# Performance work log

Hardware: AMD Instinct MI355X
Metric: run time of the kernel (lower is better)

Reference implementation:

```python
import jax, jax.numpy as jnp
import numpy as np

B, L, D = 64, 512, 128  # batch, word_len, dim


def setup_inputs() -> dict:
    key = jax.random.key(0)
    ks = jax.random.split(key, 12)
    p = lambda k, s: jax.random.normal(k, s, dtype=jnp.float32) * 0.05
    return {
        "EW": jax.random.normal(ks[0], (B, L, D), dtype=jnp.float32),
        "ES": jax.random.normal(ks[1], (B, L, D), dtype=jnp.float32),
        "WQ_w": p(ks[2], (D, D)), "WQ_b": p(ks[3], (D,)),
        "WK_w": p(ks[4], (D, D)), "WK_b": p(ks[5], (D,)),
        "UQ_w": p(ks[6], (D, D)), "UQ_b": p(ks[7], (D,)),
        "UK_w": p(ks[8], (D, D)), "UK_b": p(ks[9], (D,)),
        "V_w": p(ks[10], (D, D)), "V_b": p(ks[11], (D,)),
    }


def reference(EW, ES, WQ_w, WQ_b, WK_w, WK_b, UQ_w, UQ_b, UK_w, UK_b, V_w, V_b):
    dim = EW.shape[-1]
    word_len = EW.shape[-2]
    scale = 1.0 / (2.0 * dim ** 0.5)
    # word-level Q/K and sentence-level UQ/UK projections (torch Linear: x @ W.T + b)
    Q = (EW @ WQ_w.T + WQ_b) * scale   # [B, L, D]
    K = (EW @ WK_w.T + WK_b) * scale   # [B, L, D]
    UQ = (ES @ UQ_w.T + UQ_b) * scale  # [B, L, D]
    UK = (ES @ UK_w.T + UK_b) * scale  # [B, L, D]
    # two-term score matrix [B, L, L]
    alpha = jnp.einsum('bid,bjd->bij', Q, K) + jnp.einsum('bid,bjd->bij', UQ, UK)
    # manual exp/sum softmax exactly as in the source (no max subtraction;
    # denominator is broadcast along axis 1, faithful to unsqueeze(1))
    numerator = jnp.exp(alpha)                      # [B, L, L]
    denominator = numerator.sum(axis=-1)[:, None, :]  # [B, 1, L]
    soft = numerator / denominator                  # [B, L, L]
    value = EW @ V_w.T + V_b                        # [B, L, D]
    # faithful reinterpreting view (NOT a transpose): [B, L, D] -> [B, D, L]
    value = value.reshape(-1, dim, word_len)
    result = value @ soft                           # [B, D, L]
    return result.reshape(-1, word_len, dim)        # [B, L, D]
```

## Files before the change

kernel.cpp:

```cpp
#include <hip/hip_runtime.h>
#include <hip/hip_bf16.h>

#define NB 64
#define NL 512
#define ND 128
#define NK 256

typedef unsigned short ush;
typedef __attribute__((ext_vector_type(8))) short short8;
typedef __attribute__((ext_vector_type(16))) float f32x16;


__device__ __forceinline__ ush f2bs(float f) {
    union { __hip_bfloat16 h; ush u; } cv;
    cv.h = __float2bfloat16(f);
    return cv.u;
}
__device__ __forceinline__ short8 pack_bf8(float4 a, float4 b) {
    short8 r;
    r[0] = (short)f2bs(a.x); r[1] = (short)f2bs(a.y);
    r[2] = (short)f2bs(a.z); r[3] = (short)f2bs(a.w);
    r[4] = (short)f2bs(b.x); r[5] = (short)f2bs(b.y);
    r[6] = (short)f2bs(b.z); r[7] = (short)f2bs(b.w);
    return r;
}
__device__ __forceinline__ f32x16 zero16() {
    f32x16 z = {0.f,0.f,0.f,0.f,0.f,0.f,0.f,0.f,0.f,0.f,0.f,0.f,0.f,0.f,0.f,0.f};
    return z;
}

__global__ __launch_bounds__(256) void wconv_kernel(
    const float* __restrict__ W0, const float* __restrict__ W1,
    const float* __restrict__ W2, const float* __restrict__ W3,
    const float* __restrict__ W4, ush* __restrict__ Wb)
{
    const int m = blockIdx.y;
    const float* W = (m == 0) ? W0 : (m == 1) ? W1 : (m == 2) ? W2 : (m == 3) ? W3 : W4;
    const int e = (blockIdx.x * 256 + threadIdx.x) * 4;
    float4 v = *(const float4*)(W + e);
    ushort4 o;
    o.x = f2bs(v.x); o.y = f2bs(v.y); o.z = f2bs(v.z); o.w = f2bs(v.w);
    *(ushort4*)(Wb + m * 16384 + e) = o;
}

__global__ __launch_bounds__(256) void projqk_kernel(
    const float* __restrict__ EW, const float* __restrict__ ES,
    const ush* __restrict__ Wb,
    const float* __restrict__ b0, const float* __restrict__ b1,
    const float* __restrict__ b2, const float* __restrict__ b3,
    ush* __restrict__ QUf, ush* __restrict__ KUf)
{
    __shared__ ush Tls[4][2048];
    const int f = blockIdx.x;
    const int xcd = f & 7, loc = f >> 3;
    const int rt = xcd * 32 + (loc >> 2);
    const int m  = loc & 3;
    const int tid = threadIdx.x, w = tid >> 6, lane = tid & 63;
    const int l5 = lane & 31, hi = lane >> 5;
    const float* X = (m >= 2) ? ES : EW;
    const int rbase = rt * 128 + w * 32;

    const float* xr = X + (size_t)(rbase + l5) * ND + hi * 8;
    short8 af[8];
    #pragma unroll
    for (int ks = 0; ks < 8; ++ks)
        af[ks] = pack_bf8(*(const float4*)(xr + ks * 16),
                          *(const float4*)(xr + ks * 16 + 4));

    const ush* Wm = Wb + m * 16384;
    const float* Bp = (m == 0) ? b0 : (m == 1) ? b1 : (m == 2) ? b2 : b3;
    const float scl = 0.044194173824159216f;

    f32x16 acc[4];
    acc[0] = zero16(); acc[1] = zero16(); acc[2] = zero16(); acc[3] = zero16();
    #pragma unroll
    for (int ks = 0; ks < 8; ++ks) {
        #pragma unroll
        for (int nb = 0; nb < 4; ++nb) {
            short8 bf_ = *(const short8*)(Wm + (nb * 32 + l5) * 128 + ks * 16 + hi * 8);
            acc[nb] = __builtin_amdgcn_mfma_f32_32x32x16_bf16(af[ks], bf_, acc[nb], 0, 0, 0);
        }
    }

    char* Tc = (char*)Tls[w];
    ush* dstf = (m == 0 || m == 2) ? QUf : KUf;
    const int ko = (m >= 2) ? 8 : 0;
    const int p_g = rt * 4 + w;
    #pragma unroll
    for (int pass = 0; pass < 2; ++pass) {
        #pragma unroll
        for (int nbl = 0; nbl < 2; ++nbl) {
            const int nb = pass * 2 + nbl;
            float bias = Bp[nb * 32 + l5];
            #pragma unroll
            for (int r6 = 0; r6 < 16; ++r6) {
                int row = (r6 & 3) + 8 * (r6 >> 2) + 4 * hi;
                int boff = row * 128 + (((nbl * 32 + l5) * 2) ^ ((row & 7) << 4));
                *(ush*)(Tc + boff) = f2bs((acc[nb][r6] + bias) * scl);
            }
        }
        #pragma unroll
        for (int ks8 = 0; ks8 < 4; ++ks8) {
            int boff = l5 * 128 + ((ks8 * 32 + hi * 16) ^ ((l5 & 7) << 4));
            short8 v = *(const short8*)(Tc + boff);
            int ksg = ko + pass * 4 + ks8;
            *(short8*)(dstf + ((size_t)(p_g * 16 + ksg) * 64 + lane) * 8) = v;
        }
    }
}

__global__ __launch_bounds__(256) void projv_kernel(
    const float* __restrict__ EW, const ush* __restrict__ Wb,
    const float* __restrict__ b4, ush* __restrict__ Vbf)
{
    __shared__ ush lds[16384];
    const int f = blockIdx.x;
    const int rt = (f & 7) * 32 + (f >> 3);
    const int tid = threadIdx.x, w = tid >> 6, lane = tid & 63;
    const int l5 = lane & 31, hi = lane >> 5;
    const int rbase = rt * 128 + w * 32;

    const float* xr = EW + (size_t)(rbase + l5) * ND + hi * 8;
    short8 af[8];
    #pragma unroll
    for (int ks = 0; ks < 8; ++ks)
        af[ks] = pack_bf8(*(const float4*)(xr + ks * 16),
                          *(const float4*)(xr + ks * 16 + 4));

    const ush* Wm = Wb + 4 * 16384;
    f32x16 acc[4];
    acc[0] = zero16(); acc[1] = zero16(); acc[2] = zero16(); acc[3] = zero16();
    #pragma unroll
    for (int ks = 0; ks < 8; ++ks) {
        #pragma unroll
        for (int nb = 0; nb < 4; ++nb) {
            short8 bf_ = *(const short8*)(Wm + (nb * 32 + l5) * 128 + ks * 16 + hi * 8);
            acc[nb] = __builtin_amdgcn_mfma_f32_32x32x16_bf16(af[ks], bf_, acc[nb], 0, 0, 0);
        }
    }

    char* Lc = (char*)lds;
    #pragma unroll
    for (int nb = 0; nb < 4; ++nb) {
        float bias = b4[nb * 32 + l5];
        #pragma unroll
        for (int r6 = 0; r6 < 16; ++r6) {
            int row5 = (r6 & 3) + 8 * (r6 >> 2) + 4 * hi;
            int dl = w * 8 + (row5 >> 2);
            int lcol = (row5 & 3) * 128 + nb * 32 + l5;
            int boff = dl * 1024 + ((lcol * 2) ^ ((dl & 7) << 4));
            *(ush*)(Lc + boff) = f2bs(acc[nb][r6] + bias);
        }
    }
    __syncthreads();
    #pragma unroll
    for (int it = 0; it < 8; ++it) {
        int chunk = it * 256 + tid;
        int ks = chunk >> 6, ln = chunk & 63;
        int l5b = ln & 31, hib = ln >> 5;
        int boff = l5b * 1024 + ((ks * 32 + hib * 16) ^ ((l5b & 7) << 4));
        short8 v = *(const short8*)(Lc + boff);
        *(short8*)(Vbf + ((size_t)(rt * 32 + ks) * 64 + ln) * 8) = v;
    }
}

__global__ __launch_bounds__(256) void alpha_kernel(
    const ush* __restrict__ QUf, const ush* __restrict__ KUf,
    ush* __restrict__ Nf, float* __restrict__ dPart)
{
    __shared__ float red[4][2][16];
    __shared__ ush TlsA[4][2048];
    const int f = blockIdx.x;
    const int xcd = f & 7, loc = f >> 3;
    const int b  = xcd * 8 + (loc >> 5);
    const int rt = (loc >> 1) & 15;
    const int ch = loc & 1;
    const int tid = threadIdx.x, w = tid >> 6, lane = tid & 63;
    const int l5 = lane & 31, hi = lane >> 5;
    const ush* Qb = QUf + (size_t)b * 131072;
    const ush* Kb = KUf + (size_t)b * 131072;
    ush* Nfb = Nf + (size_t)b * 262144;

    const ush* qp = Qb + (size_t)rt * 8192 + lane * 8;
    const int cpg0 = ch * 8 + w * 2;

    f32x16 a0[2], a1[2];
    a0[0] = zero16(); a0[1] = zero16(); a1[0] = zero16(); a1[1] = zero16();
    #pragma unroll
    for (int ks = 0; ks < 16; ks += 2) {
        short8 aqa = *(const short8*)(qp + ks * 512);
        short8 aqb = *(const short8*)(qp + (ks + 1) * 512);
        #pragma unroll
        for (int cp = 0; cp < 2; ++cp) {
            const ush* kp = Kb + (size_t)((cpg0 + cp) * 16) * 512 + lane * 8;
            a0[cp] = __builtin_amdgcn_mfma_f32_32x32x16_bf16(aqa,
                         *(const short8*)(kp + ks * 512), a0[cp], 0, 0, 0);
            a1[cp] = __builtin_amdgcn_mfma_f32_32x32x16_bf16(aqb,
                         *(const short8*)(kp + (ks + 1) * 512), a1[cp], 0, 0, 0);
        }
    }

    float rs[16];
    #pragma unroll
    for (int r6 = 0; r6 < 16; ++r6) rs[r6] = 0.f;
    char* Tc = (char*)TlsA[w];
    #pragma unroll
    for (int cp = 0; cp < 2; ++cp) {
        const int cpg = cpg0 + cp;
        float e[16];
        #pragma unroll
        for (int r6 = 0; r6 < 16; ++r6) {
            e[r6] = __expf(a0[cp][r6] + a1[cp][r6]);
            rs[r6] += e[r6];
        }
        #pragma unroll
        for (int q = 0; q < 8; ++q) {
            int r6 = q * 2;
            int r = (r6 & 3) + 8 * (r6 >> 2) + 4 * hi;
            unsigned int pk = (unsigned int)f2bs(e[r6])
                            | ((unsigned int)f2bs(e[r6 + 1]) << 16);
            *(unsigned int*)(Tc + l5 * 128 + ((r * 2) ^ ((l5 & 7) << 4))) = pk;
        }
        #pragma unroll
        for (int ksl = 0; ksl < 2; ++ksl) {
            short8 v = *(const short8*)(Tc + l5 * 128 +
                           (((ksl * 16 + hi * 8) * 2) ^ ((l5 & 7) << 4)));
            int ksg = rt * 2 + ksl;
            *(short8*)(Nfb + ((size_t)(cpg * 32 + ksg) * 64 + lane) * 8) = v;
        }
    }

    #pragma unroll
    for (int mk = 1; mk <= 16; mk <<= 1)
        #pragma unroll
        for (int r6 = 0; r6 < 16; ++r6) rs[r6] += __shfl_xor(rs[r6], mk, 32);
    if (l5 == 0)
        #pragma unroll
        for (int r6 = 0; r6 < 16; ++r6) red[w][hi][r6] = rs[r6];
    __syncthreads();
    if (tid < 32) {
        int t = tid;
        int hh = (t >> 2) & 1, r6 = (t & 3) + 4 * (t >> 3);
        float s = red[0][hh][r6] + red[1][hh][r6] + red[2][hh][r6] + red[3][hh][r6];
        dPart[((size_t)b * 2 + ch) * NL + rt * 32 + t] = s;
    }
}

__global__ __launch_bounds__(256) void pv_kernel(
    const ush* __restrict__ Vbf, const ush* __restrict__ Nf,
    const float* __restrict__ dPart, float* __restrict__ out)
{
    const int f = blockIdx.x;
    const int xcd = f & 7, loc = f >> 3;
    const int b  = xcd * 8 + (loc >> 4);
    const int ct = loc & 15;
    const int tid = threadIdx.x, w = tid >> 6, lane = tid & 63;
    const int l5 = lane & 31, hi = lane >> 5;
    const ush* Vbb = Vbf + (size_t)b * 65536;
    const ush* Nfb = Nf + (size_t)b * 262144;
    const size_t obase = (size_t)b * (ND * NL);

    const ush* vp = Vbb + (size_t)w * 16384 + lane * 8;
    const ush* np = Nfb + (size_t)ct * 16384 + lane * 8;

    f32x16 acc0 = zero16(), acc1 = zero16();
    #pragma unroll
    for (int ks = 0; ks < 32; ks += 2) {
        acc0 = __builtin_amdgcn_mfma_f32_32x32x16_bf16(*(const short8*)(vp + ks * 512),
                   *(const short8*)(np + ks * 512), acc0, 0, 0, 0);
        acc1 = __builtin_amdgcn_mfma_f32_32x32x16_bf16(*(const short8*)(vp + (ks + 1) * 512),
                   *(const short8*)(np + (ks + 1) * 512), acc1, 0, 0, 0);
    }
    f32x16 acc = acc0 + acc1;
    const int c0 = ct * 32;
    float rd = 1.0f / (dPart[((size_t)b * 2 + 0) * NL + c0 + l5]
                     + dPart[((size_t)b * 2 + 1) * NL + c0 + l5]);
    #pragma unroll
    for (int r6 = 0; r6 < 16; ++r6) {
        int d = w * 32 + (r6 & 3) + 8 * (r6 >> 2) + 4 * hi;
        out[obase + (size_t)d * NL + c0 + l5] = acc[r6] * rd;
    }
}

__global__ __launch_bounds__(256) void fused_kernel(
    const ush* __restrict__ QUf, const ush* __restrict__ KUf,
    const ush* __restrict__ Vbf, float* __restrict__ out)
{
    __shared__ ush Pt[32 * 136];
    __shared__ float red[128];
    __shared__ float rdenS[32];
    const int f = blockIdx.x;
    const int xcd = f & 7, loc = f >> 3;
    const int b  = xcd * 8 + (loc >> 4);
    const int ct = loc & 15, c0 = ct * 32;
    const int tid = threadIdx.x, w = tid >> 6, lane = tid & 63;
    const int l5 = lane & 31, hi = lane >> 5;
    const ush* Qb  = QUf + (size_t)b * 131072;
    const ush* Kb  = KUf + (size_t)b * 131072;
    const ush* Vbb = Vbf + (size_t)b * 65536;
    const size_t obase = (size_t)b * (ND * NL);

    {
        short8 aq[16];
        const ush* qp = Qb + (size_t)ct * 8192 + lane * 8;
        #pragma unroll
        for (int ks = 0; ks < 16; ++ks) aq[ks] = *(const short8*)(qp + ks * 512);
        float rs[16];
        #pragma unroll
        for (int r = 0; r < 16; ++r) rs[r] = 0.f;
        #pragma unroll
        for (int t = 0; t < 4; ++t) {
            const ush* kp = Kb + (size_t)(w * 4 + t) * 8192 + lane * 8;
            f32x16 a0 = zero16(), a1 = zero16();
            #pragma unroll
            for (int ks = 0; ks < 16; ks += 2) {
                a0 = __builtin_amdgcn_mfma_f32_32x32x16_bf16(aq[ks],     *(const short8*)(kp + ks * 512),       a0, 0, 0, 0);
                a1 = __builtin_amdgcn_mfma_f32_32x32x16_bf16(aq[ks + 1], *(const short8*)(kp + (ks + 1) * 512), a1, 0, 0, 0);
            }
            #pragma unroll
            for (int r = 0; r < 16; ++r) rs[r] += __expf(a0[r] + a1[r]);
        }
        #pragma unroll
        for (int mk = 1; mk <= 16; mk <<= 1)
            #pragma unroll
            for (int r = 0; r < 16; ++r) rs[r] += __shfl_xor(rs[r], mk, 32);
        if (l5 == 0)
            #pragma unroll
            for (int r = 0; r < 16; ++r) red[(w * 2 + hi) * 16 + r] = rs[r];
    }
    __syncthreads();
    if (tid < 32) {
        int c = tid;
        int h2 = (c >> 2) & 1, r = (c & 3) + 4 * (c >> 3);
        float s = 0.f;
        #pragma unroll
        for (int kh = 0; kh < 4; ++kh) s += red[(kh * 2 + h2) * 16 + r];
        rdenS[c] = 1.0f / s;
    }
    __syncthreads();

    const int p2 = w;
    const float rden = rdenS[l5];
    const ush* kp2 = Kb + (size_t)ct * 8192 + lane * 8;
    f32x16 oA = zero16(), oB = zero16();

    for (int it = 0; it < 4; ++it) {
        if (it) __syncthreads();
        const ush* qp2 = Qb + (size_t)(it * 4 + p2) * 8192 + lane * 8;
        f32x16 s0 = zero16(), s1 = zero16();
        #pragma unroll
        for (int ks = 0; ks < 16; ks += 2) {
            s0 = __builtin_amdgcn_mfma_f32_32x32x16_bf16(*(const short8*)(qp2 + ks * 512),
                                                         *(const short8*)(kp2 + ks * 512),       s0, 0, 0, 0);
            s1 = __builtin_amdgcn_mfma_f32_32x32x16_bf16(*(const short8*)(qp2 + (ks + 1) * 512),
                                                         *(const short8*)(kp2 + (ks + 1) * 512), s1, 0, 0, 0);
        }
        #pragma unroll
        for (int q = 0; q < 4; ++q) {
            ushort4 pv;
            pv.x = f2bs(__expf(s0[q * 4 + 0] + s1[q * 4 + 0]) * rden);
            pv.y = f2bs(__expf(s0[q * 4 + 1] + s1[q * 4 + 1]) * rden);
            pv.z = f2bs(__expf(s0[q * 4 + 2] + s1[q * 4 + 2]) * rden);
            pv.w = f2bs(__expf(s0[q * 4 + 3] + s1[q * 4 + 3]) * rden);
            int boff = l5 * 272 + (((p2 * 32 + q * 8 + hi * 4) * 2) ^ ((l5 & 7) << 4));
            *(ushort4*)((char*)Pt + boff) = pv;
        }
        __syncthreads();
        #pragma unroll
        for (int j = 0; j < 8; j += 2) {
            short8 va0 = *(const short8*)(Vbb + ((size_t)(p2 * 32 + it * 8 + j) * 64 + lane) * 8);
            short8 pb0 = *(const short8*)((char*)Pt + l5 * 272 + (((j * 16 + hi * 8) * 2) ^ ((l5 & 7) << 4)));
            oA = __builtin_amdgcn_mfma_f32_32x32x16_bf16(va0, pb0, oA, 0, 0, 0);
            short8 va1 = *(const short8*)(Vbb + ((size_t)(p2 * 32 + it * 8 + j + 1) * 64 + lane) * 8);
            short8 pb1 = *(const short8*)((char*)Pt + l5 * 272 + ((((j + 1) * 16 + hi * 8) * 2) ^ ((l5 & 7) << 4)));
            oB = __builtin_amdgcn_mfma_f32_32x32x16_bf16(va1, pb1, oB, 0, 0, 0);
        }
    }
    f32x16 oacc = oA + oB;
    #pragma unroll
    for (int r = 0; r < 16; ++r) {
        int d = p2 * 32 + (r & 3) + 8 * (r >> 2) + 4 * hi;
        out[obase + (size_t)d * NL + c0 + l5] = oacc[r];
    }
}

extern "C" void kernel_launch(void* const* d_in, const int* in_sizes, int n_in,
                              void* d_out, int out_size, void* d_ws, size_t ws_size,
                              hipStream_t stream)
{
    const float* EW   = (const float*)d_in[0];
    const float* ES   = (const float*)d_in[1];
    const float* WQ_w = (const float*)d_in[2];
    const float* WQ_b = (const float*)d_in[3];
    const float* WK_w = (const float*)d_in[4];
    const float* WK_b = (const float*)d_in[5];
    const float* UQ_w = (const float*)d_in[6];
    const float* UQ_b = (const float*)d_in[7];
    const float* UK_w = (const float*)d_in[8];
    const float* UK_b = (const float*)d_in[9];
    const float* V_w  = (const float*)d_in[10];
    const float* V_b  = (const float*)d_in[11];

    if (ws_size < (size_t)41 * 1024 * 1024) return;

    char* ws = (char*)d_ws;
    ush* QUf = (ush*)ws;
    ush* KUf = (ush*)(ws + (size_t)16 * 1024 * 1024);
    ush* Vbf = (ush*)(ws + (size_t)32 * 1024 * 1024);
    ush* Wb  = (ush*)(ws + (size_t)40 * 1024 * 1024);
    float* dPart = (float*)(ws + (size_t)40 * 1024 * 1024 + 512 * 1024);
    ush* Nf  = (ush*)(ws + (size_t)41 * 1024 * 1024);
    float* outp = (float*)d_out;

    wconv_kernel<<<dim3(16, 5), 256, 0, stream>>>(WQ_w, WK_w, UQ_w, UK_w, V_w, Wb);
    projqk_kernel<<<1024, 256, 0, stream>>>(EW, ES, Wb,
                                            WQ_b, WK_b, UQ_b, UK_b, QUf, KUf);
    projv_kernel<<<256, 256, 0, stream>>>(EW, Wb, V_b, Vbf);
    if (ws_size >= (size_t)74 * 1024 * 1024) {
        alpha_kernel<<<2048, 256, 0, stream>>>(QUf, KUf, Nf, dPart);
        pv_kernel<<<1024, 256, 0, stream>>>(Vbf, Nf, dPart, outp);
    } else {
        fused_kernel<<<1024, 256, 0, stream>>>(QUf, KUf, Vbf, outp);
    }
}
```

Before: 80.86 us.

## Pre-convert EW/ES to bf16 once and prefetch K fragments in alpha kernel

Adds an xconv kernel that converts EW and ES to bf16 once into workspace, so projqk (which reads each input twice across its Q/K blocks) and projv read half-size bf16 rows instead of converting fp32 repeatedly. Separately, the alpha kernel's score loop now software-pipelines K-fragment global loads one step ahead of the MFMAs. The new path needs a larger workspace (92 MiB) and adds an extra kernel launch plus an extra fp32 read and bf16 write pass over the inputs.

After: 89.53 us. +10.7%, slower.

```diff
diff --git a/kernel.cpp b/kernel.cpp
--- a/kernel.cpp
+++ b/kernel.cpp
@@ -43,8 +43,22 @@
     *(ushort4*)(Wb + m * 16384 + e) = o;
 }
 
+__global__ __launch_bounds__(256) void xconv_kernel(
+    const float* __restrict__ EW, const float* __restrict__ ES,
+    ush* __restrict__ EWb, ush* __restrict__ ESb)
+{
+    const int m = blockIdx.y;
+    const float* X = m ? ES : EW;
+    ush* Xb = m ? ESb : EWb;
+    const int e = (blockIdx.x * 256 + threadIdx.x) * 8;
+    float4 a = *(const float4*)(X + e);
+    float4 b = *(const float4*)(X + e + 4);
+    *(short8*)(Xb + e) = pack_bf8(a, b);
+}
+
 __global__ __launch_bounds__(256) void projqk_kernel(
     const float* __restrict__ EW, const float* __restrict__ ES,
+    const ush* __restrict__ EWb, const ush* __restrict__ ESb, int useb,
     const ush* __restrict__ Wb,
     const float* __restrict__ b0, const float* __restrict__ b1,
     const float* __restrict__ b2, const float* __restrict__ b3,
@@ -57,15 +71,20 @@
     const int m  = loc & 3;
     const int tid = threadIdx.x, w = tid >> 6, lane = tid & 63;
     const int l5 = lane & 31, hi = lane >> 5;
-    const float* X = (m >= 2) ? ES : EW;
     const int rbase = rt * 128 + w * 32;
 
-    const float* xr = X + (size_t)(rbase + l5) * ND + hi * 8;
     short8 af[8];
-    #pragma unroll
-    for (int ks = 0; ks < 8; ++ks)
-        af[ks] = pack_bf8(*(const float4*)(xr + ks * 16),
-                          *(const float4*)(xr + ks * 16 + 4));
+    if (useb) {
+        const ush* xr = (m >= 2 ? ESb : EWb) + (size_t)(rbase + l5) * ND + hi * 8;
+        #pragma unroll
+        for (int ks = 0; ks < 8; ++ks) af[ks] = *(const short8*)(xr + ks * 16);
+    } else {
+        const float* xr = (m >= 2 ? ES : EW) + (size_t)(rbase + l5) * ND + hi * 8;
+        #pragma unroll
+        for (int ks = 0; ks < 8; ++ks)
+            af[ks] = pack_bf8(*(const float4*)(xr + ks * 16),
+                              *(const float4*)(xr + ks * 16 + 4));
+    }
 
     const ush* Wm = Wb + m * 16384;
     const float* Bp = (m == 0) ? b0 : (m == 1) ? b1 : (m == 2) ? b2 : b3;
@@ -110,7 +129,8 @@
 }
 
 __global__ __launch_bounds__(256) void projv_kernel(
-    const float* __restrict__ EW, const ush* __restrict__ Wb,
+    const float* __restrict__ EW, const ush* __restrict__ EWb, int useb,
+    const ush* __restrict__ Wb,
     const float* __restrict__ b4, ush* __restrict__ Vbf)
 {
     __shared__ ush lds[16384];
@@ -120,12 +140,18 @@
     const int l5 = lane & 31, hi = lane >> 5;
     const int rbase = rt * 128 + w * 32;
 
-    const float* xr = EW + (size_t)(rbase + l5) * ND + hi * 8;
     short8 af[8];
-    #pragma unroll
-    for (int ks = 0; ks < 8; ++ks)
-        af[ks] = pack_bf8(*(const float4*)(xr + ks * 16),
-                          *(const float4*)(xr + ks * 16 + 4));
+    if (useb) {
+        const ush* xr = EWb + (size_t)(rbase + l5) * ND + hi * 8;
+        #pragma unroll
+        for (int ks = 0; ks < 8; ++ks) af[ks] = *(const short8*)(xr + ks * 16);
+    } else {
+        const float* xr = EW + (size_t)(rbase + l5) * ND + hi * 8;
+        #pragma unroll
+        for (int ks = 0; ks < 8; ++ks)
+            af[ks] = pack_bf8(*(const float4*)(xr + ks * 16),
+                              *(const float4*)(xr + ks * 16 + 4));
+    }
 
     const ush* Wm = Wb + 4 * 16384;
     f32x16 acc[4];
@@ -183,21 +209,32 @@
 
     const ush* qp = Qb + (size_t)rt * 8192 + lane * 8;
     const int cpg0 = ch * 8 + w * 2;
+    const ush* kpp0 = Kb + (size_t)((cpg0 + 0) * 16) * 512 + lane * 8;
+    const ush* kpp1 = Kb + (size_t)((cpg0 + 1) * 16) * 512 + lane * 8;
 
     f32x16 a0[2], a1[2];
     a0[0] = zero16(); a0[1] = zero16(); a1[0] = zero16(); a1[1] = zero16();
+
+    short8 c0a = *(const short8*)(kpp0);
+    short8 c0b = *(const short8*)(kpp0 + 512);
+    short8 c1a = *(const short8*)(kpp1);
+    short8 c1b = *(const short8*)(kpp1 + 512);
     #pragma unroll
     for (int ks = 0; ks < 16; ks += 2) {
+        short8 n0a, n0b, n1a, n1b;
+        if (ks < 14) {
+            n0a = *(const short8*)(kpp0 + (ks + 2) * 512);
+            n0b = *(const short8*)(kpp0 + (ks + 3) * 512);
+            n1a = *(const short8*)(kpp1 + (ks + 2) * 512);
+            n1b = *(const short8*)(kpp1 + (ks + 3) * 512);
+        }
         short8 aqa = *(const short8*)(qp + ks * 512);
         short8 aqb = *(const short8*)(qp + (ks + 1) * 512);
-        #pragma unroll
-        for (int cp = 0; cp < 2; ++cp) {
-            const ush* kp = Kb + (size_t)((cpg0 + cp) * 16) * 512 + lane * 8;
-            a0[cp] = __builtin_amdgcn_mfma_f32_32x32x16_bf16(aqa,
-                         *(const short8*)(kp + ks * 512), a0[cp], 0, 0, 0);
-            a1[cp] = __builtin_amdgcn_mfma_f32_32x32x16_bf16(aqb,
-                         *(const short8*)(kp + (ks + 1) * 512), a1[cp], 0, 0, 0);
-        }
+        a0[0] = __builtin_amdgcn_mfma_f32_32x32x16_bf16(aqa, c0a, a0[0], 0, 0, 0);
+        a1[0] = __builtin_amdgcn_mfma_f32_32x32x16_bf16(aqb, c0b, a1[0], 0, 0, 0);
+        a0[1] = __builtin_amdgcn_mfma_f32_32x32x16_bf16(aqa, c1a, a0[1], 0, 0, 0);
+        a1[1] = __builtin_amdgcn_mfma_f32_32x32x16_bf16(aqb, c1b, a1[1], 0, 0, 0);
+        if (ks < 14) { c0a = n0a; c0b = n0b; c1a = n1a; c1b = n1b; }
     }
 
     float rs[16];
@@ -410,12 +447,18 @@
     ush* Wb  = (ush*)(ws + (size_t)40 * 1024 * 1024);
     float* dPart = (float*)(ws + (size_t)40 * 1024 * 1024 + 512 * 1024);
     ush* Nf  = (ush*)(ws + (size_t)41 * 1024 * 1024);
+    ush* EWb = (ush*)(ws + (size_t)74 * 1024 * 1024);
+    ush* ESb = (ush*)(ws + (size_t)83 * 1024 * 1024);
     float* outp = (float*)d_out;
 
+    const int useb = (ws_size >= (size_t)92 * 1024 * 1024) ? 1 : 0;
+
     wconv_kernel<<<dim3(16, 5), 256, 0, stream>>>(WQ_w, WK_w, UQ_w, UK_w, V_w, Wb);
-    projqk_kernel<<<1024, 256, 0, stream>>>(EW, ES, Wb,
+    if (useb)
+        xconv_kernel<<<dim3(2048, 2), 256, 0, stream>>>(EW, ES, EWb, ESb);
+    projqk_kernel<<<1024, 256, 0, stream>>>(EW, ES, EWb, ESb, useb, Wb,
                                             WQ_b, WK_b, UQ_b, UK_b, QUf, KUf);
-    projv_kernel<<<256, 256, 0, stream>>>(EW, Wb, V_b, Vbf);
+    projv_kernel<<<256, 256, 0, stream>>>(EW, EWb, useb, Wb, V_b, Vbf);
     if (ws_size >= (size_t)74 * 1024 * 1024) {
         alpha_kernel<<<2048, 256, 0, stream>>>(QUf, KUf, Nf, dPart);
         pv_kernel<<<1024, 256, 0, stream>>>(Vbf, Nf, dPart, outp);
```
